# Kernel optimization log

Measured on AMD Instinct MI355X. Metric: run time of the kernel, lower is better.

The kernel has to match this reference:

```python
import jax, jax.numpy as jnp
import numpy as np

D_MODEL = 1024
NUM_HEADS = 16
D_K = D_MODEL // NUM_HEADS


def setup_inputs() -> dict:
    key = jax.random.key(0)
    ks = jax.random.split(key, 11)
    B, S = 4, 2048
    scale = 1.0 / np.sqrt(D_MODEL)
    inp = {
        'query': jax.random.normal(ks[0], (B, S, D_MODEL), jnp.float32),
        'key': jax.random.normal(ks[1], (B, S, D_MODEL), jnp.float32),
        'value': jax.random.normal(ks[2], (B, S, D_MODEL), jnp.float32),
        'Wq': jax.random.normal(ks[3], (D_MODEL, D_MODEL), jnp.float32) * scale,
        'bq': jnp.zeros((D_MODEL,), jnp.float32),
        'Wk': jax.random.normal(ks[4], (D_MODEL, D_MODEL), jnp.float32) * scale,
        'bk': jnp.zeros((D_MODEL,), jnp.float32),
        'Wv': jax.random.normal(ks[5], (D_MODEL, D_MODEL), jnp.float32) * scale,
        'bv': jnp.zeros((D_MODEL,), jnp.float32),
        'Wo': jax.random.normal(ks[6], (D_MODEL, D_MODEL), jnp.float32) * scale,
        'bo': jnp.zeros((D_MODEL,), jnp.float32),
    }
    return inp


def _split_heads(x):
    # [B, S, D] -> [B, H, S, d_k]
    B, S, _ = x.shape
    return x.reshape(B, S, NUM_HEADS, D_K).transpose(0, 2, 1, 3)


def reference(query, key, value, Wq, bq, Wk, bk, Wv, bv, Wo, bo):
    # torch nn.Linear: y = x @ W.T + b
    q = _split_heads(query @ Wq.T + bq)   # [B,H,Sq,dk]
    k = _split_heads(key @ Wk.T + bk)     # [B,H,Sk,dk]
    v = _split_heads(value @ Wv.T + bv)   # [B,H,Sk,dk]
    scores = jnp.einsum('bhqd,bhkd->bhqk', q, k) / jnp.sqrt(jnp.float32(D_K))
    attn = jax.nn.softmax(scores, axis=-1)
    out = jnp.einsum('bhqk,bhkd->bhqd', attn, v)  # [B,H,Sq,dk]
    B, H, Sq, dk = out.shape
    out = out.transpose(0, 2, 1, 3).reshape(B, Sq, D_MODEL)
    return out @ Wo.T + bo
```

## Files before the change

kernel.cpp:

```cpp
#include <hip/hip_runtime.h>

typedef short bf16x8 __attribute__((ext_vector_type(8)));
typedef float f32x4 __attribute__((ext_vector_type(4)));
typedef unsigned short u16;

#define S_LEN 2048
#define DM 1024
#define NH 16
#define DK 64
#define BHD ((size_t)S_LEN * DK)

#define QSCALE 0.18033688011112042f

static __device__ __forceinline__ u16 f2bf(float f) {
  union { float f; unsigned u; } x; x.f = f;
  unsigned r = x.u + 0x7FFFu + ((x.u >> 16) & 1u);
  return (u16)(r >> 16);
}

static __device__ __forceinline__ void gload_lds16(const u16* g, u16* l) {
  __builtin_amdgcn_global_load_lds(
      (const __attribute__((address_space(1))) unsigned int*)g,
      (__attribute__((address_space(3))) unsigned int*)l, 16, 0, 0);
}

__global__ __launch_bounds__(256) void conv_w(
    const float* __restrict__ Wq, const float* __restrict__ Wk,
    const float* __restrict__ Wv, const float* __restrict__ Wo,
    u16* __restrict__ wb) {
  const int b = blockIdx.x;
  const int wsel = b >> 10;
  const float* s = (wsel == 0) ? Wq : (wsel == 1) ? Wk : (wsel == 2) ? Wv : Wo;
  const float sc = (wsel == 0) ? QSCALE : 1.0f;
  u16* d = wb + (size_t)wsel * 1048576;
  int i = (b & 1023) * 256 + threadIdx.x;
  float4 vv = ((const float4*)s)[i];
  ushort4 h;
  h.x = f2bf(vv.x * sc); h.y = f2bf(vv.y * sc);
  h.z = f2bf(vv.z * sc); h.w = f2bf(vv.w * sc);
  ((ushort4*)d)[i] = h;
}

#define GSTAGE(DST, SRC)                                                          \
  {                                                                               \
    _Pragma("unroll") for (int j = 0; j < 4; ++j) {                               \
      gload_lds16((SRC) + (size_t)(j * 32 + (w << 3) + (l >> 3)) * 1024 +         \
                      (size_t)(((l & 7) ^ (l >> 3)) * 8),                         \
                  (DST) + (j * 256 + w * 64) * 8);                                \
    }                                                                             \
  }

#define ASTAGE_LOAD(R, SRCF, K0)                                                  \
  {                                                                               \
    _Pragma("unroll") for (int j = 0; j < 4; ++j) {                               \
      const int r_ = j * 32 + (t >> 3);                                           \
      const int g_ = (t & 7) ^ (r_ & 7);                                          \
      const float* p_ = (SRCF) + (size_t)(m0 + r_) * 1024 + (K0) + g_ * 8;        \
      R[j][0] = *(const float4*)(p_);                                             \
      R[j][1] = *(const float4*)(p_ + 4);                                         \
    }                                                                             \
  }
#define ASTAGE_WRITE(DST, R)                                                      \
  {                                                                               \
    _Pragma("unroll") for (int j = 0; j < 4; ++j) {                               \
      unsigned u0, u1, u2, u3;                                                    \
      asm("v_cvt_pk_bf16_f32 %0, %1, %2" : "=v"(u0) : "v"(R[j][0].x), "v"(R[j][0].y)); \
      asm("v_cvt_pk_bf16_f32 %0, %1, %2" : "=v"(u1) : "v"(R[j][0].z), "v"(R[j][0].w)); \
      asm("v_cvt_pk_bf16_f32 %0, %1, %2" : "=v"(u2) : "v"(R[j][1].x), "v"(R[j][1].y)); \
      asm("v_cvt_pk_bf16_f32 %0, %1, %2" : "=v"(u3) : "v"(R[j][1].z), "v"(R[j][1].w)); \
      uint4 pk_; pk_.x = u0; pk_.y = u1; pk_.z = u2; pk_.w = u3;                  \
      *(uint4*)((DST) + (size_t)(t + j * 256) * 8) = pk_;                         \
    }                                                                             \
  }

__global__ __launch_bounds__(256) void proj_gemm(
    const float* __restrict__ qf32, const float* __restrict__ kf32,
    const float* __restrict__ vf32, const u16* __restrict__ wb,
    const float* __restrict__ bq, const float* __restrict__ bk, const float* __restrict__ bv,
    u16* __restrict__ qws, u16* __restrict__ kws, u16* __restrict__ vws)
{
  __shared__ u16 Al[2][128 * 64];
  __shared__ u16 Bl[2][128 * 64];
  const int z = blockIdx.z;
  const float* Xf = (z == 0) ? qf32 : (z == 1) ? kf32 : vf32;
  const u16* Wb = wb + (size_t)z * 1048576;
  const float* bias = (z == 0) ? bq : (z == 1) ? bk : bv;
  const float bscale = (z == 0) ? QSCALE : 1.0f;

  const int t = threadIdx.x;
  const int l = t & 63, w = t >> 6;
  const int lr = l & 15, lg = l >> 4;
  const int wm = w >> 1, wn = w & 1;
  const int m0 = blockIdx.x * 128, n0 = blockIdx.y * 128;
  const int sxr = lr & 7;

  f32x4 acc[4][4] = {};
  float4 areg[4][2];

  ASTAGE_LOAD(areg, Xf, 0)
  GSTAGE(&Bl[0][0], Wb + (size_t)n0 * 1024)
  ASTAGE_WRITE(&Al[0][0], areg)

  for (int i = 0; i < 16; ++i) {
    __syncthreads();
    if (i < 15) {
      ASTAGE_LOAD(areg, Xf, (i + 1) * 64)
      GSTAGE(&Bl[(i + 1) & 1][0], Wb + (size_t)n0 * 1024 + (i + 1) * 64)
    }
    const u16* Ab_ = &Al[i & 1][0];
    const u16* Bb_ = &Bl[i & 1][0];

    bf16x8 a[4][2], b[4][2];
#pragma unroll
    for (int mi = 0; mi < 4; ++mi) {
      const u16* rp = Ab_ + (wm * 64 + mi * 16 + lr) * 64;
      a[mi][0] = *(const bf16x8*)(rp + ((lg ^ sxr) * 8));
      a[mi][1] = *(const bf16x8*)(rp + (((4 + lg) ^ sxr) * 8));
    }
#pragma unroll
    for (int ni = 0; ni < 4; ++ni) {
      const u16* rp = Bb_ + (wn * 64 + ni * 16 + lr) * 64;
      b[ni][0] = *(const bf16x8*)(rp + ((lg ^ sxr) * 8));
      b[ni][1] = *(const bf16x8*)(rp + (((4 + lg) ^ sxr) * 8));
    }
    __builtin_amdgcn_s_setprio(1);
#pragma unroll
    for (int mi = 0; mi < 4; ++mi)
#pragma unroll
      for (int ni = 0; ni < 4; ++ni) {
        acc[mi][ni] = __builtin_amdgcn_mfma_f32_16x16x32_bf16(a[mi][0], b[ni][0], acc[mi][ni], 0, 0, 0);
        acc[mi][ni] = __builtin_amdgcn_mfma_f32_16x16x32_bf16(a[mi][1], b[ni][1], acc[mi][ni], 0, 0, 0);
      }
    __builtin_amdgcn_s_setprio(0);

    if (i < 15) ASTAGE_WRITE(&Al[(i + 1) & 1][0], areg)
  }

#pragma unroll
  for (int mi = 0; mi < 4; ++mi) {
#pragma unroll
    for (int ni = 0; ni < 4; ++ni) {
#pragma unroll
      for (int r = 0; r < 4; ++r) {
        int m = m0 + wm * 64 + mi * 16 + lg * 4 + r;
        int n = n0 + wn * 64 + ni * 16 + lr;
        float y = acc[mi][ni][r] + bias[n] * bscale;
        u16 h = f2bf(y);
        int b_ = m >> 11, s = m & 2047, hh = n >> 6, d = n & 63;
        size_t head = (size_t)(b_ * NH + hh);
        if (z == 0)      qws[head * BHD + (size_t)s * DK + d] = h;
        else if (z == 1) kws[head * BHD + (size_t)s * DK + d] = h;
        else             vws[head * BHD + (size_t)d * S_LEN + s] = h;
      }
    }
  }
}

__global__ __launch_bounds__(256) void oproj_gemm(
    const u16* __restrict__ Ab, const u16* __restrict__ Wob,
    const float* __restrict__ bo, float* __restrict__ out)
{
  __shared__ u16 Al[2][128 * 64];
  __shared__ u16 Bl[2][128 * 64];
  const int t = threadIdx.x;
  const int l = t & 63, w = t >> 6;
  const int lr = l & 15, lg = l >> 4;
  const int wm = w >> 1, wn = w & 1;
  const int m0 = blockIdx.x * 128, n0 = blockIdx.y * 128;
  const int sxr = lr & 7;

  f32x4 acc[4][4] = {};

  GSTAGE(&Al[0][0], Ab + (size_t)m0 * 1024)
  GSTAGE(&Bl[0][0], Wob + (size_t)n0 * 1024)

  for (int i = 0; i < 16; ++i) {
    __syncthreads();
    if (i < 15) {
      GSTAGE(&Al[(i + 1) & 1][0], Ab + (size_t)m0 * 1024 + (i + 1) * 64)
      GSTAGE(&Bl[(i + 1) & 1][0], Wob + (size_t)n0 * 1024 + (i + 1) * 64)
    }
    const u16* Ab_ = &Al[i & 1][0];
    const u16* Bb_ = &Bl[i & 1][0];

    bf16x8 a[4][2], b[4][2];
#pragma unroll
    for (int mi = 0; mi < 4; ++mi) {
      const u16* rp = Ab_ + (wm * 64 + mi * 16 + lr) * 64;
      a[mi][0] = *(const bf16x8*)(rp + ((lg ^ sxr) * 8));
      a[mi][1] = *(const bf16x8*)(rp + (((4 + lg) ^ sxr) * 8));
    }
#pragma unroll
    for (int ni = 0; ni < 4; ++ni) {
      const u16* rp = Bb_ + (wn * 64 + ni * 16 + lr) * 64;
      b[ni][0] = *(const bf16x8*)(rp + ((lg ^ sxr) * 8));
      b[ni][1] = *(const bf16x8*)(rp + (((4 + lg) ^ sxr) * 8));
    }
    __builtin_amdgcn_s_setprio(1);
#pragma unroll
    for (int mi = 0; mi < 4; ++mi)
#pragma unroll
      for (int ni = 0; ni < 4; ++ni) {
        acc[mi][ni] = __builtin_amdgcn_mfma_f32_16x16x32_bf16(a[mi][0], b[ni][0], acc[mi][ni], 0, 0, 0);
        acc[mi][ni] = __builtin_amdgcn_mfma_f32_16x16x32_bf16(a[mi][1], b[ni][1], acc[mi][ni], 0, 0, 0);
      }
    __builtin_amdgcn_s_setprio(0);
  }

#pragma unroll
  for (int mi = 0; mi < 4; ++mi) {
#pragma unroll
    for (int ni = 0; ni < 4; ++ni) {
#pragma unroll
      for (int r = 0; r < 4; ++r) {
        int m = m0 + wm * 64 + mi * 16 + lg * 4 + r;
        int n = n0 + wn * 64 + ni * 16 + lr;
        out[(size_t)m * DM + n] = acc[mi][ni][r] + bo[n];
      }
    }
  }
}

__global__ __launch_bounds__(256, 4) void attn_kernel(
    const u16* __restrict__ qh, const u16* __restrict__ kh,
    const u16* __restrict__ vt, u16* __restrict__ aout)
{
  __shared__ u16 KT[2][64 * 64];
  __shared__ u16 VT[2][64 * 64];

  const int t = threadIdx.x;
  const int l = t & 63, w = t >> 6;
  const int lr = l & 15, lg = l >> 4;

  const int bid = blockIdx.x;
  const int logical = (bid & 7) * 128 + (bid >> 3);
  const int bh = logical >> 4;
  const int qb = (logical & 15) * 128 + w * 32;

  const u16* qp = qh + (size_t)bh * BHD;
  const u16* kp = kh + (size_t)bh * BHD;
  const u16* vp = vt + (size_t)bh * BHD;
  const int sx = lr & 7;

  const int srow = t >> 3;
  const int scolS = (t & 7) ^ (srow & 7);

  bf16x8 qf[2][2];
#pragma unroll
  for (int qi = 0; qi < 2; ++qi)
#pragma unroll
    for (int c = 0; c < 2; ++c)
      qf[qi][c] = *(const bf16x8*)(qp + (size_t)(qb + qi * 16 + lr) * DK + c * 32 + lg * 8);

  bf16x8 onesf;
#pragma unroll
  for (int e = 0; e < 8; ++e) onesf[e] = (short)0x3F80;

  f32x4 acc[4][2] = {};
  f32x4 acc_l[2] = {};

#define STAGE(B, KV)                                                                  \
  {                                                                                   \
    _Pragma("unroll") for (int j = 0; j < 2; ++j) {                                   \
      gload_lds16(kp + (size_t)((KV) + j * 32 + srow) * DK + scolS * 8,               \
                  &KT[B][j * 2048 + w * 512]);                                        \
      gload_lds16(vp + (size_t)(j * 32 + srow) * S_LEN + (KV) + scolS * 8,            \
                  &VT[B][j * 2048 + w * 512]);                                        \
    }                                                                                 \
  }

  STAGE(0, 0)

  for (int i = 0; i < 32; ++i) {
    __syncthreads();
    if (i < 31) STAGE((i + 1) & 1, (i + 1) * 64)

    const u16* Kb = &KT[i & 1][0];
    const u16* Vb = &VT[i & 1][0];

    f32x4 sc[4][2] = {};
    __builtin_amdgcn_s_setprio(1);
#pragma unroll
    for (int ct = 0; ct < 4; ++ct) {
      bf16x8 k0 = *(const bf16x8*)(Kb + (ct * 16 + lr) * 64 + ((lg ^ sx) * 8));
      bf16x8 k1 = *(const bf16x8*)(Kb + (ct * 16 + lr) * 64 + (((4 + lg) ^ sx) * 8));
      sc[ct][0] = __builtin_amdgcn_mfma_f32_16x16x32_bf16(k0, qf[0][0], sc[ct][0], 0, 0, 0);
      sc[ct][0] = __builtin_amdgcn_mfma_f32_16x16x32_bf16(k1, qf[0][1], sc[ct][0], 0, 0, 0);
      sc[ct][1] = __builtin_amdgcn_mfma_f32_16x16x32_bf16(k0, qf[1][0], sc[ct][1], 0, 0, 0);
      sc[ct][1] = __builtin_amdgcn_mfma_f32_16x16x32_bf16(k1, qf[1][1], sc[ct][1], 0, 0, 0);
    }
    __builtin_amdgcn_s_setprio(0);

    unsigned cpk[2][4][2];
#pragma unroll
    for (int qi = 0; qi < 2; ++qi) {
#pragma unroll
      for (int ct = 0; ct < 4; ++ct) {
        float p0 = __builtin_amdgcn_exp2f(sc[ct][qi][0]);
        float p1 = __builtin_amdgcn_exp2f(sc[ct][qi][1]);
        float p2 = __builtin_amdgcn_exp2f(sc[ct][qi][2]);
        float p3 = __builtin_amdgcn_exp2f(sc[ct][qi][3]);
        asm("v_cvt_pk_bf16_f32 %0, %1, %2" : "=v"(cpk[qi][ct][0]) : "v"(p0), "v"(p1));
        asm("v_cvt_pk_bf16_f32 %0, %1, %2" : "=v"(cpk[qi][ct][1]) : "v"(p2), "v"(p3));
      }
    }

    bf16x8 pf[2][2];
#pragma unroll
    for (int qi = 0; qi < 2; ++qi)
#pragma unroll
      for (int kk = 0; kk < 2; ++kk) {
        unsigned a0 = cpk[qi][2 * kk][0], b0 = cpk[qi][2 * kk + 1][0];
        unsigned a1 = cpk[qi][2 * kk][1], b1 = cpk[qi][2 * kk + 1][1];
        asm("v_permlane32_swap_b32 %0, %1" : "+v"(a0), "+v"(b0));
        asm("v_permlane16_swap_b32 %0, %1" : "+v"(a0), "+v"(b0));
        asm("v_permlane32_swap_b32 %0, %1" : "+v"(a1), "+v"(b1));
        asm("v_permlane16_swap_b32 %0, %1" : "+v"(a1), "+v"(b1));
        union { unsigned u[4]; bf16x8 v; } tmp;
        tmp.u[0] = a0; tmp.u[1] = a1; tmp.u[2] = b0; tmp.u[3] = b1;
        pf[qi][kk] = tmp.v;
      }

    __builtin_amdgcn_s_setprio(1);
    acc_l[0] = __builtin_amdgcn_mfma_f32_16x16x32_bf16(pf[0][0], onesf, acc_l[0], 0, 0, 0);
    acc_l[0] = __builtin_amdgcn_mfma_f32_16x16x32_bf16(pf[0][1], onesf, acc_l[0], 0, 0, 0);
    acc_l[1] = __builtin_amdgcn_mfma_f32_16x16x32_bf16(pf[1][0], onesf, acc_l[1], 0, 0, 0);
    acc_l[1] = __builtin_amdgcn_mfma_f32_16x16x32_bf16(pf[1][1], onesf, acc_l[1], 0, 0, 0);
#pragma unroll
    for (int ni = 0; ni < 4; ++ni) {
      bf16x8 vf0 = *(const bf16x8*)(Vb + (ni * 16 + lr) * 64 + ((lg ^ sx) * 8));
      bf16x8 vf1 = *(const bf16x8*)(Vb + (ni * 16 + lr) * 64 + (((4 + lg) ^ sx) * 8));
      acc[ni][0] = __builtin_amdgcn_mfma_f32_16x16x32_bf16(pf[0][0], vf0, acc[ni][0], 0, 0, 0);
      acc[ni][0] = __builtin_amdgcn_mfma_f32_16x16x32_bf16(pf[0][1], vf1, acc[ni][0], 0, 0, 0);
      acc[ni][1] = __builtin_amdgcn_mfma_f32_16x16x32_bf16(pf[1][0], vf0, acc[ni][1], 0, 0, 0);
      acc[ni][1] = __builtin_amdgcn_mfma_f32_16x16x32_bf16(pf[1][1], vf1, acc[ni][1], 0, 0, 0);
    }
    __builtin_amdgcn_s_setprio(0);
  }
#undef STAGE

  const int b_ = bh >> 4, hh = bh & 15;
#pragma unroll
  for (int qi = 0; qi < 2; ++qi) {
#pragma unroll
    for (int r = 0; r < 4; ++r) {
      float inv = 1.0f / acc_l[qi][r];
      int s = qb + qi * 16 + lg * 4 + r;
#pragma unroll
      for (int ni = 0; ni < 4; ++ni)
        aout[((size_t)(b_ * S_LEN + s)) * DM + hh * DK + ni * 16 + lr] =
            f2bf(acc[ni][qi][r] * inv);
    }
  }
}

extern "C" void kernel_launch(void* const* d_in, const int* in_sizes, int n_in,
                              void* d_out, int out_size, void* d_ws, size_t ws_size,
                              hipStream_t stream) {
  (void)in_sizes; (void)n_in; (void)out_size; (void)ws_size;
  const float* q  = (const float*)d_in[0];
  const float* k  = (const float*)d_in[1];
  const float* v  = (const float*)d_in[2];
  const float* Wq = (const float*)d_in[3];
  const float* bq = (const float*)d_in[4];
  const float* Wk = (const float*)d_in[5];
  const float* bk = (const float*)d_in[6];
  const float* Wv = (const float*)d_in[7];
  const float* bv = (const float*)d_in[8];
  const float* Wo = (const float*)d_in[9];
  const float* bo = (const float*)d_in[10];
  float* out = (float*)d_out;

  u16* qws = (u16*)d_ws;
  u16* kws = qws + (size_t)8388608;
  u16* vws = kws + (size_t)8388608;
  u16* aws = vws + (size_t)8388608;
  u16* wb  = aws + (size_t)8388608;

  conv_w<<<dim3(4096), dim3(256), 0, stream>>>(Wq, Wk, Wv, Wo, wb);

  proj_gemm<<<dim3(64, 8, 3), dim3(256), 0, stream>>>(q, k, v, wb, bq, bk, bv,
                                                      qws, kws, vws);

  attn_kernel<<<dim3(1024), dim3(256), 0, stream>>>(qws, kws, vws, aws);

  oproj_gemm<<<dim3(64, 8), dim3(256), 0, stream>>>(aws, wb + 3145728, bo, out);
}
```

Baseline: 197.5 us.

## Halve GEMM K-tile to 32 and prefetch activations two stages ahead

```diff
diff --git a/kernel.cpp b/kernel.cpp
--- a/kernel.cpp
+++ b/kernel.cpp
@@ -41,35 +41,33 @@
   ((ushort4*)d)[i] = h;
 }
 
-#define GSTAGE(DST, SRC)                                                          \
+
+#define GSTAGE32(DST, SRC, K0)                                                    \
   {                                                                               \
-    _Pragma("unroll") for (int j = 0; j < 4; ++j) {                               \
-      gload_lds16((SRC) + (size_t)(j * 32 + (w << 3) + (l >> 3)) * 1024 +         \
-                      (size_t)(((l & 7) ^ (l >> 3)) * 8),                         \
-                  (DST) + (j * 256 + w * 64) * 8);                                \
+    _Pragma("unroll") for (int j = 0; j < 2; ++j) {                               \
+      gload_lds16((SRC) + (size_t)(j * 64 + srow) * 1024 + (K0) + schnk * 8,      \
+                  (DST) + j * 2048 + w * 512);                                    \
     }                                                                             \
   }
 
-#define ASTAGE_LOAD(R, SRCF, K0)                                                  \
+#define ASTAGE_LOAD32(R, SRCF, K0)                                                \
   {                                                                               \
-    _Pragma("unroll") for (int j = 0; j < 4; ++j) {                               \
-      const int r_ = j * 32 + (t >> 3);                                           \
-      const int g_ = (t & 7) ^ (r_ & 7);                                          \
-      const float* p_ = (SRCF) + (size_t)(m0 + r_) * 1024 + (K0) + g_ * 8;        \
+    _Pragma("unroll") for (int j = 0; j < 2; ++j) {                               \
+      const float* p_ = (SRCF) + (size_t)(m0 + j * 64 + srow) * 1024 + (K0) + schnk * 8; \
       R[j][0] = *(const float4*)(p_);                                             \
       R[j][1] = *(const float4*)(p_ + 4);                                         \
     }                                                                             \
   }
-#define ASTAGE_WRITE(DST, R)                                                      \
+#define ASTAGE_WRITE32(DST, R)                                                    \
   {                                                                               \
-    _Pragma("unroll") for (int j = 0; j < 4; ++j) {                               \
+    _Pragma("unroll") for (int j = 0; j < 2; ++j) {                               \
       unsigned u0, u1, u2, u3;                                                    \
       asm("v_cvt_pk_bf16_f32 %0, %1, %2" : "=v"(u0) : "v"(R[j][0].x), "v"(R[j][0].y)); \
       asm("v_cvt_pk_bf16_f32 %0, %1, %2" : "=v"(u1) : "v"(R[j][0].z), "v"(R[j][0].w)); \
       asm("v_cvt_pk_bf16_f32 %0, %1, %2" : "=v"(u2) : "v"(R[j][1].x), "v"(R[j][1].y)); \
       asm("v_cvt_pk_bf16_f32 %0, %1, %2" : "=v"(u3) : "v"(R[j][1].z), "v"(R[j][1].w)); \
       uint4 pk_; pk_.x = u0; pk_.y = u1; pk_.z = u2; pk_.w = u3;                  \
-      *(uint4*)((DST) + (size_t)(t + j * 256) * 8) = pk_;                         \
+      *(uint4*)((DST) + (size_t)(j * 2048 + t * 8)) = pk_;                        \
     }                                                                             \
   }
 
@@ -79,8 +77,8 @@
     const float* __restrict__ bq, const float* __restrict__ bk, const float* __restrict__ bv,
     u16* __restrict__ qws, u16* __restrict__ kws, u16* __restrict__ vws)
 {
-  __shared__ u16 Al[2][128 * 64];
-  __shared__ u16 Bl[2][128 * 64];
+  __shared__ u16 Al[2][128 * 32];
+  __shared__ u16 Bl[2][128 * 32];
   const int z = blockIdx.z;
   const float* Xf = (z == 0) ? qf32 : (z == 1) ? kf32 : vf32;
   const u16* Wb = wb + (size_t)z * 1048576;
@@ -92,48 +90,43 @@
   const int lr = l & 15, lg = l >> 4;
   const int wm = w >> 1, wn = w & 1;
   const int m0 = blockIdx.x * 128, n0 = blockIdx.y * 128;
-  const int sxr = lr & 7;
+  const int sx4 = lr & 3;
+  const int srow = t >> 2;
+  const int schnk = (t & 3) ^ (srow & 3);
 
   f32x4 acc[4][4] = {};
-  float4 areg[4][2];
-
-  ASTAGE_LOAD(areg, Xf, 0)
-  GSTAGE(&Bl[0][0], Wb + (size_t)n0 * 1024)
-  ASTAGE_WRITE(&Al[0][0], areg)
-
-  for (int i = 0; i < 16; ++i) {
+  float4 areg[2][2];
+
+  ASTAGE_LOAD32(areg, Xf, 0)
+  GSTAGE32(&Bl[0][0], Wb + (size_t)n0 * 1024, 0)
+  ASTAGE_WRITE32(&Al[0][0], areg)
+  ASTAGE_LOAD32(areg, Xf, 32)
+
+  for (int i = 0; i < 32; ++i) {
     __syncthreads();
-    if (i < 15) {
-      ASTAGE_LOAD(areg, Xf, (i + 1) * 64)
-      GSTAGE(&Bl[(i + 1) & 1][0], Wb + (size_t)n0 * 1024 + (i + 1) * 64)
-    }
+    if (i < 31) {
+      ASTAGE_WRITE32(&Al[(i + 1) & 1][0], areg)
+      GSTAGE32(&Bl[(i + 1) & 1][0], Wb + (size_t)n0 * 1024, (i + 1) * 32)
+    }
+    if (i < 30) ASTAGE_LOAD32(areg, Xf, (i + 2) * 32)
+
     const u16* Ab_ = &Al[i & 1][0];
     const u16* Bb_ = &Bl[i & 1][0];
 
-    bf16x8 a[4][2], b[4][2];
-#pragma unroll
-    for (int mi = 0; mi < 4; ++mi) {
-      const u16* rp = Ab_ + (wm * 64 + mi * 16 + lr) * 64;
-      a[mi][0] = *(const bf16x8*)(rp + ((lg ^ sxr) * 8));
-      a[mi][1] = *(const bf16x8*)(rp + (((4 + lg) ^ sxr) * 8));
-    }
-#pragma unroll
-    for (int ni = 0; ni < 4; ++ni) {
-      const u16* rp = Bb_ + (wn * 64 + ni * 16 + lr) * 64;
-      b[ni][0] = *(const bf16x8*)(rp + ((lg ^ sxr) * 8));
-      b[ni][1] = *(const bf16x8*)(rp + (((4 + lg) ^ sxr) * 8));
-    }
+    bf16x8 a[4], b[4];
+#pragma unroll
+    for (int mi = 0; mi < 4; ++mi)
+      a[mi] = *(const bf16x8*)(Ab_ + (wm * 64 + mi * 16 + lr) * 32 + ((lg ^ sx4) * 8));
+#pragma unroll
+    for (int ni = 0; ni < 4; ++ni)
+      b[ni] = *(const bf16x8*)(Bb_ + (wn * 64 + ni * 16 + lr) * 32 + ((lg ^ sx4) * 8));
     __builtin_amdgcn_s_setprio(1);
 #pragma unroll
     for (int mi = 0; mi < 4; ++mi)
 #pragma unroll
-      for (int ni = 0; ni < 4; ++ni) {
-        acc[mi][ni] = __builtin_amdgcn_mfma_f32_16x16x32_bf16(a[mi][0], b[ni][0], acc[mi][ni], 0, 0, 0);
-        acc[mi][ni] = __builtin_amdgcn_mfma_f32_16x16x32_bf16(a[mi][1], b[ni][1], acc[mi][ni], 0, 0, 0);
-      }
+      for (int ni = 0; ni < 4; ++ni)
+        acc[mi][ni] = __builtin_amdgcn_mfma_f32_16x16x32_bf16(a[mi], b[ni], acc[mi][ni], 0, 0, 0);
     __builtin_amdgcn_s_setprio(0);
-
-    if (i < 15) ASTAGE_WRITE(&Al[(i + 1) & 1][0], areg)
   }
 
 #pragma unroll
@@ -160,50 +153,44 @@
     const u16* __restrict__ Ab, const u16* __restrict__ Wob,
     const float* __restrict__ bo, float* __restrict__ out)
 {
-  __shared__ u16 Al[2][128 * 64];
-  __shared__ u16 Bl[2][128 * 64];
+  __shared__ u16 Al[2][128 * 32];
+  __shared__ u16 Bl[2][128 * 32];
   const int t = threadIdx.x;
   const int l = t & 63, w = t >> 6;
   const int lr = l & 15, lg = l >> 4;
   const int wm = w >> 1, wn = w & 1;
   const int m0 = blockIdx.x * 128, n0 = blockIdx.y * 128;
-  const int sxr = lr & 7;
+  const int sx4 = lr & 3;
+  const int srow = t >> 2;
+  const int schnk = (t & 3) ^ (srow & 3);
 
   f32x4 acc[4][4] = {};
 
-  GSTAGE(&Al[0][0], Ab + (size_t)m0 * 1024)
-  GSTAGE(&Bl[0][0], Wob + (size_t)n0 * 1024)
-
-  for (int i = 0; i < 16; ++i) {
+  GSTAGE32(&Al[0][0], Ab + (size_t)m0 * 1024, 0)
+  GSTAGE32(&Bl[0][0], Wob + (size_t)n0 * 1024, 0)
+
+  for (int i = 0; i < 32; ++i) {
     __syncthreads();
-    if (i < 15) {
-      GSTAGE(&Al[(i + 1) & 1][0], Ab + (size_t)m0 * 1024 + (i + 1) * 64)
-      GSTAGE(&Bl[(i + 1) & 1][0], Wob + (size_t)n0 * 1024 + (i + 1) * 64)
+    if (i < 31) {
+      GSTAGE32(&Al[(i + 1) & 1][0], Ab + (size_t)m0 * 1024, (i + 1) * 32)
+      GSTAGE32(&Bl[(i + 1) & 1][0], Wob + (size_t)n0 * 1024, (i + 1) * 32)
     }
     const u16* Ab_ = &Al[i & 1][0];
     const u16* Bb_ = &Bl[i & 1][0];
 
-    bf16x8 a[4][2], b[4][2];
-#pragma unroll
-    for (int mi = 0; mi < 4; ++mi) {
-      const u16* rp = Ab_ + (wm * 64 + mi * 16 + lr) * 64;
-      a[mi][0] = *(const bf16x8*)(rp + ((lg ^ sxr) * 8));
-      a[mi][1] = *(const bf16x8*)(rp + (((4 + lg) ^ sxr) * 8));
-    }
-#pragma unroll
-    for (int ni = 0; ni < 4; ++ni) {
-      const u16* rp = Bb_ + (wn * 64 + ni * 16 + lr) * 64;
-      b[ni][0] = *(const bf16x8*)(rp + ((lg ^ sxr) * 8));
-      b[ni][1] = *(const bf16x8*)(rp + (((4 + lg) ^ sxr) * 8));
-    }
+    bf16x8 a[4], b[4];
+#pragma unroll
+    for (int mi = 0; mi < 4; ++mi)
+      a[mi] = *(const bf16x8*)(Ab_ + (wm * 64 + mi * 16 + lr) * 32 + ((lg ^ sx4) * 8));
+#pragma unroll
+    for (int ni = 0; ni < 4; ++ni)
+      b[ni] = *(const bf16x8*)(Bb_ + (wn * 64 + ni * 16 + lr) * 32 + ((lg ^ sx4) * 8));
     __builtin_amdgcn_s_setprio(1);
 #pragma unroll
     for (int mi = 0; mi < 4; ++mi)
 #pragma unroll
-      for (int ni = 0; ni < 4; ++ni) {
-        acc[mi][ni] = __builtin_amdgcn_mfma_f32_16x16x32_bf16(a[mi][0], b[ni][0], acc[mi][ni], 0, 0, 0);
-        acc[mi][ni] = __builtin_amdgcn_mfma_f32_16x16x32_bf16(a[mi][1], b[ni][1], acc[mi][ni], 0, 0, 0);
-      }
+      for (int ni = 0; ni < 4; ++ni)
+        acc[mi][ni] = __builtin_amdgcn_mfma_f32_16x16x32_bf16(a[mi], b[ni], acc[mi][ni], 0, 0, 0);
     __builtin_amdgcn_s_setprio(0);
   }
 
```

New measurement: 199.7 us. About the same (+1.1%).
